# Kernel tuning notes

Measured on AMD Instinct MI355X. Metric: run time of the kernel, lower is better.

Reference implementation:

```python
import jax, jax.numpy as jnp
import numpy as np

B, S, D, E, K, O = 32, 2048, 1024, 16, 4, 1024


def setup_inputs() -> dict:
    key = jax.random.key(0)
    ks = jax.random.split(key, 9)
    sc = 0.02
    return {
        "x": jax.random.normal(ks[0], (B, S, D), dtype=jnp.float32),
        "Wg": jax.random.normal(ks[1], (D, E), dtype=jnp.float32) * sc,
        "bg": jnp.zeros((E,), dtype=jnp.float32),
        "W1": jax.random.normal(ks[2], (E, K * D, O), dtype=jnp.float32) * sc,
        "b1": jnp.zeros((E, O), dtype=jnp.float32),
        "W2": jax.random.normal(ks[3], (E, O, O), dtype=jnp.float32) * sc,
        "b2": jnp.zeros((E, O), dtype=jnp.float32),
        "W3": jax.random.normal(ks[4], (E, O, O), dtype=jnp.float32) * sc,
        "b3": jnp.zeros((E, O), dtype=jnp.float32),
    }


def reference(x, Wg, bg, W1, b1, W2, b2, W3, b3):
    b, s, d = x.shape
    e = Wg.shape[1]
    k = W1.shape[1] // d
    # gate logits [B,S,E]; softmax over the TOKEN axis (dim=-2 in torch)
    logits = jnp.einsum('bsd,de->bse', x, Wg) + bg
    probs = jax.nn.softmax(logits, axis=-2)          # [B,S,E]
    # top-k tokens per expert (torch.topk over dim=-2)
    vals, idx = jax.lax.top_k(probs.transpose(0, 2, 1), k)  # [B,E,k]
    # gather selected tokens: [B,E,k,D]
    tok = jnp.take_along_axis(x[:, None, :, :], idx[..., None], axis=2)
    # weight by gate prob, concat k tokens -> [B,E,k*D]
    inp = (tok * vals[..., None]).reshape(b, e, k * d)
    # per-expert 3-layer MLP as grouped GEMMs
    h = jax.nn.relu(jnp.einsum('bei,eio->beo', inp, W1) + b1)
    h = jax.nn.relu(jnp.einsum('beo,eop->bep', h, W2) + b2)
    out = jnp.einsum('beo,eop->bep', h, W3) + b3
    return out  # [B,E,O]
```

## Files before the change

kernel.cpp:

```cpp
#include <hip/hip_runtime.h>
#include <hip/hip_bf16.h>
#include <math.h>

constexpr int B = 32, S = 2048, D = 1024, E = 16, TK = 4, O = 1024;
constexpr int KD = TK * D;
constexpr int KS = 8;

__global__ __launch_bounds__(256) void k_logits(
    const float* __restrict__ x, const float* __restrict__ Wg,
    const float* __restrict__ bg, float* __restrict__ logitsT) {
  int row = blockIdx.x * 256 + threadIdx.x;
  int b = row / S, s = row % S;
  const float* xr = x + (size_t)row * D;
  float acc[E];
#pragma unroll
  for (int e = 0; e < E; e++) acc[e] = 0.f;
  for (int k = 0; k < D; k += 4) {
    float4 xv = *(const float4*)(xr + k);
    const float* w0 = Wg + (size_t)k * E;
#pragma unroll
    for (int e = 0; e < E; e++) {
      acc[e] += xv.x * w0[e] + xv.y * w0[E + e] + xv.z * w0[2 * E + e] +
                xv.w * w0[3 * E + e];
    }
  }
#pragma unroll
  for (int e = 0; e < E; e++)
    logitsT[((size_t)b * E + e) * S + s] = acc[e] + bg[e];
}

__global__ __launch_bounds__(256) void k_topk(
    const float* __restrict__ logitsT, int* __restrict__ tIdx,
    float* __restrict__ tVal) {
  int be = blockIdx.x;
  const float* lrow = logitsT + (size_t)be * S;
  __shared__ float sv[S];
  __shared__ float red[256];
  __shared__ int redi[256];
  int t = threadIdx.x;
  for (int i = t; i < S; i += 256) sv[i] = lrow[i];
  __syncthreads();
  float m = -1e30f;
  for (int i = t; i < S; i += 256) m = fmaxf(m, sv[i]);
  red[t] = m;
  __syncthreads();
  for (int off = 128; off > 0; off >>= 1) {
    if (t < off) red[t] = fmaxf(red[t], red[t + off]);
    __syncthreads();
  }
  float gmax = red[0];
  __syncthreads();
  float se = 0.f;
  for (int i = t; i < S; i += 256) se += expf(sv[i] - gmax);
  red[t] = se;
  __syncthreads();
  for (int off = 128; off > 0; off >>= 1) {
    if (t < off) red[t] += red[t + off];
    __syncthreads();
  }
  float sumexp = red[0];
  __syncthreads();
  for (int j = 0; j < 4; j++) {
    float bv = -1e30f;
    int bi = S;
    for (int i = t; i < S; i += 256) {
      float v = sv[i];
      if (v > bv || (v == bv && i < bi)) { bv = v; bi = i; }
    }
    red[t] = bv;
    redi[t] = bi;
    __syncthreads();
    for (int off = 128; off > 0; off >>= 1) {
      if (t < off) {
        float v2 = red[t + off];
        int i2 = redi[t + off];
        if (v2 > red[t] || (v2 == red[t] && i2 < redi[t])) {
          red[t] = v2;
          redi[t] = i2;
        }
      }
      __syncthreads();
    }
    if (t == 0) {
      tIdx[be * TK + j] = redi[0];
      tVal[be * TK + j] = expf(red[0] - gmax) / sumexp;
      sv[redi[0]] = -1e30f;
    }
    __syncthreads();
  }
}

__global__ __launch_bounds__(256) void k_gather(
    const float* __restrict__ x, const int* __restrict__ tIdx,
    const float* __restrict__ tVal, float* __restrict__ inpT) {
  int ej = blockIdx.x;
  int e = ej / TK, j = ej % TK;
  int d0 = blockIdx.y * 256;
  __shared__ float st[32][257];
  int tid = threadIdx.x;
  int dt = tid % 64;
  int bq = tid / 64;
  for (int bi = 0; bi < 8; bi++) {
    int b = bq * 8 + bi;
    int row = tIdx[(b * E + e) * TK + j];
    float v = tVal[(b * E + e) * TK + j];
    float4 xv = *(const float4*)(x + ((size_t)b * S + row) * D + d0 + dt * 4);
    st[b][dt * 4 + 0] = xv.x * v;
    st[b][dt * 4 + 1] = xv.y * v;
    st[b][dt * 4 + 2] = xv.z * v;
    st[b][dt * 4 + 3] = xv.w * v;
  }
  __syncthreads();
  size_t base = ((size_t)e * TK + j) * D + d0;
  for (int c = 0; c < 32; c++) {
    int idx = c * 256 + tid;
    int drel = idx / 32, b = idx % 32;
    inpT[(base + drel) * 32 + b] = st[b][drel];
  }
}

template <int KC>
__global__ __launch_bounds__(64) void k_gemm_part(
    const float* __restrict__ AT,
    const float* __restrict__ W,
    float* __restrict__ part,
    int Ktot) {
  int e = blockIdx.x, nt = blockIdx.y, ks = blockIdx.z;
  int n = nt * 64 + threadIdx.x;
  int k0 = ks * KC;
  const float* a = AT + ((size_t)e * Ktot + k0) * 32;
  const float* w = W + ((size_t)e * Ktot + k0) * O + n;
  float acc[32];
#pragma unroll
  for (int m = 0; m < 32; m++) acc[m] = 0.f;
#pragma unroll 4
  for (int k = 0; k < KC; k++) {
    float bv = w[(size_t)k * O];
    const float* ar = a + k * 32;
#pragma unroll
    for (int m = 0; m < 32; m++) acc[m] += ar[m] * bv;
  }
  float4* po4 = (float4*)(part + (((size_t)ks * E + e) * O + n) * 32);
#pragma unroll
  for (int q = 0; q < 8; q++)
    po4[q] = make_float4(acc[4 * q], acc[4 * q + 1], acc[4 * q + 2], acc[4 * q + 3]);
}

__global__ __launch_bounds__(256) void k_reduce_act(
    const float* __restrict__ part, const float* __restrict__ bias,
    float* __restrict__ outT, int relu) {
  size_t g = (size_t)blockIdx.x * 256 + threadIdx.x;
  const size_t stride4 = (size_t)E * O * 32 / 4;
  const float4* p4 = (const float4*)part;
  float4 s = p4[g];
#pragma unroll
  for (int ks = 1; ks < KS; ks++) {
    float4 v = p4[(size_t)ks * stride4 + g];
    s.x += v.x; s.y += v.y; s.z += v.z; s.w += v.w;
  }
  size_t el = g * 4;
  int n = (int)((el / 32) % O);
  int e = (int)(el / ((size_t)32 * O));
  float bv = bias[e * O + n];
  s.x += bv; s.y += bv; s.z += bv; s.w += bv;
  if (relu) {
    s.x = fmaxf(s.x, 0.f); s.y = fmaxf(s.y, 0.f);
    s.z = fmaxf(s.z, 0.f); s.w = fmaxf(s.w, 0.f);
  }
  ((float4*)outT)[g] = s;
}

__global__ __launch_bounds__(256) void k_final(
    const float* __restrict__ part, const float* __restrict__ bias,
    float* __restrict__ out) {
  int e = blockIdx.x;
  int o0 = blockIdx.y * 64;
  __shared__ float sd[64][33];
  int tid = threadIdx.x;
  const size_t stride = (size_t)E * O * 32;
  for (int c = 0; c < 8; c++) {
    int idx = c * 256 + tid;
    int orel = idx / 32, b = idx % 32;
    size_t off = ((size_t)e * O + o0 + orel) * 32 + b;
    float s = part[off];
#pragma unroll
    for (int ks = 1; ks < KS; ks++) s += part[(size_t)ks * stride + off];
    sd[orel][b] = s + bias[e * O + o0 + orel];
  }
  __syncthreads();
  for (int c = 0; c < 8; c++) {
    int idx = c * 256 + tid;
    int b = idx / 64, orr = idx % 64;
    out[((size_t)b * E + e) * O + o0 + orr] = sd[orr][b];
  }
}

extern "C" void kernel_launch(void* const* d_in, const int* in_sizes, int n_in,
                              void* d_out, int out_size, void* d_ws,
                              size_t ws_size, hipStream_t stream) {
  (void)in_sizes; (void)n_in; (void)out_size; (void)ws_size;
  const float* x  = (const float*)d_in[0];
  const float* Wg = (const float*)d_in[1];
  const float* bg = (const float*)d_in[2];
  const float* W1 = (const float*)d_in[3];
  const float* b1 = (const float*)d_in[4];
  const float* W2 = (const float*)d_in[5];
  const float* b2 = (const float*)d_in[6];
  const float* W3 = (const float*)d_in[7];
  const float* b3 = (const float*)d_in[8];
  float* out = (float*)d_out;

  char* ws = (char*)d_ws;
  float* logitsT = (float*)ws;
  int*   tIdx    = (int*)(ws + (4u << 20));
  float* tVal    = (float*)(ws + (4u << 20) + (8u << 10));
  float* inpT    = (float*)(ws + (4u << 20) + (64u << 10));
  float* part    = (float*)(ws + (12u << 20) + (64u << 10));
  float* h1T     = (float*)(ws + (28u << 20) + (64u << 10));
  float* h2T     = (float*)(ws + (30u << 20) + (64u << 10));

  k_logits<<<B * S / 256, 256, 0, stream>>>(x, Wg, bg, logitsT);
  k_topk<<<B * E, 256, 0, stream>>>(logitsT, tIdx, tVal);
  k_gather<<<dim3(E * TK, D / 256), 256, 0, stream>>>(x, tIdx, tVal, inpT);
  k_gemm_part<KD / KS><<<dim3(E, O / 64, KS), 64, 0, stream>>>(inpT, W1, part, KD);
  k_reduce_act<<<(E * O * 32 / 4) / 256, 256, 0, stream>>>(part, b1, h1T, 1);
  k_gemm_part<O / KS><<<dim3(E, O / 64, KS), 64, 0, stream>>>(h1T, W2, part, O);
  k_reduce_act<<<(E * O * 32 / 4) / 256, 256, 0, stream>>>(part, b2, h2T, 1);
  k_gemm_part<O / KS><<<dim3(E, O / 64, KS), 64, 0, stream>>>(h2T, W3, part, O);
  k_final<<<dim3(E, O / 64), 256, 0, stream>>>(part, b3, out);
}
```

Before: 847.6 us.

## Split logits K across waves and retile expert GEMM for vector weight loads

The gate-logit kernel now gives each of four waves a quarter of the feature dimension for 64 rows. It batches eight float4 loads of x per iteration and reduces the partial sums through shared memory. This raises memory-level parallelism on the large x read. The expert GEMM moves from 64-thread blocks, where each thread handled one output column and all 32 batch rows, to 256-thread blocks. Each thread now computes 4 columns by 8 rows using float4 weight loads unrolled by eight, which quarters the grid size and changes occupancy and register use.

```diff
diff --git a/kernel.cpp b/kernel.cpp
--- a/kernel.cpp
+++ b/kernel.cpp
@@ -9,24 +9,43 @@
 __global__ __launch_bounds__(256) void k_logits(
     const float* __restrict__ x, const float* __restrict__ Wg,
     const float* __restrict__ bg, float* __restrict__ logitsT) {
-  int row = blockIdx.x * 256 + threadIdx.x;
-  int b = row / S, s = row % S;
-  const float* xr = x + (size_t)row * D;
+  int tid = threadIdx.x;
+  int lane = tid & 63;
+  int wid = __builtin_amdgcn_readfirstlane(tid >> 6);
+  int row0 = blockIdx.x * 64;
+  int row = row0 + lane;
+  const float* xr = x + (size_t)row * D + wid * 256;
+  const float* wg = Wg + (size_t)wid * 256 * E;
   float acc[E];
 #pragma unroll
   for (int e = 0; e < E; e++) acc[e] = 0.f;
-  for (int k = 0; k < D; k += 4) {
-    float4 xv = *(const float4*)(xr + k);
-    const float* w0 = Wg + (size_t)k * E;
-#pragma unroll
-    for (int e = 0; e < E; e++) {
-      acc[e] += xv.x * w0[e] + xv.y * w0[E + e] + xv.z * w0[2 * E + e] +
-                xv.w * w0[3 * E + e];
-    }
-  }
-#pragma unroll
-  for (int e = 0; e < E; e++)
-    logitsT[((size_t)b * E + e) * S + s] = acc[e] + bg[e];
+  for (int it = 0; it < 64; it += 8) {
+    float4 xv[8];
+#pragma unroll
+    for (int u = 0; u < 8; u++)
+      xv[u] = *(const float4*)(xr + (it + u) * 4);
+#pragma unroll
+    for (int u = 0; u < 8; u++) {
+      const float* w0 = wg + (size_t)(it + u) * 4 * E;
+#pragma unroll
+      for (int e = 0; e < E; e++)
+        acc[e] += xv[u].x * w0[e] + xv[u].y * w0[E + e] +
+                  xv[u].z * w0[2 * E + e] + xv[u].w * w0[3 * E + e];
+    }
+  }
+  __shared__ float red[4][64][17];
+#pragma unroll
+  for (int e = 0; e < E; e++) red[wid][lane][e] = acc[e];
+  __syncthreads();
+  int b = row0 >> 11;
+  int s0 = row0 & (S - 1);
+#pragma unroll
+  for (int i = 0; i < 4; i++) {
+    int e = wid + i * 4;
+    float v = red[0][lane][e] + red[1][lane][e] + red[2][lane][e] +
+              red[3][lane][e] + bg[e];
+    logitsT[((size_t)b * E + e) * S + s0 + lane] = v;
+  }
 }
 
 __global__ __launch_bounds__(256) void k_topk(
@@ -120,30 +139,50 @@
 }
 
 template <int KC>
-__global__ __launch_bounds__(64) void k_gemm_part(
+__global__ __launch_bounds__(256) void k_gemm_part(
     const float* __restrict__ AT,
     const float* __restrict__ W,
     float* __restrict__ part,
     int Ktot) {
   int e = blockIdx.x, nt = blockIdx.y, ks = blockIdx.z;
-  int n = nt * 64 + threadIdx.x;
+  int tid = threadIdx.x;
+  int lane = tid & 63;
+  int m0 = __builtin_amdgcn_readfirstlane((tid >> 6) * 8);
+  int n0 = nt * 256 + lane * 4;
   int k0 = ks * KC;
-  const float* a = AT + ((size_t)e * Ktot + k0) * 32;
-  const float* w = W + ((size_t)e * Ktot + k0) * O + n;
-  float acc[32];
-#pragma unroll
-  for (int m = 0; m < 32; m++) acc[m] = 0.f;
-#pragma unroll 4
-  for (int k = 0; k < KC; k++) {
-    float bv = w[(size_t)k * O];
-    const float* ar = a + k * 32;
-#pragma unroll
-    for (int m = 0; m < 32; m++) acc[m] += ar[m] * bv;
-  }
-  float4* po4 = (float4*)(part + (((size_t)ks * E + e) * O + n) * 32);
-#pragma unroll
-  for (int q = 0; q < 8; q++)
-    po4[q] = make_float4(acc[4 * q], acc[4 * q + 1], acc[4 * q + 2], acc[4 * q + 3]);
+  const float* a = AT + ((size_t)e * Ktot + k0) * 32 + m0;
+  const float* w = W + ((size_t)e * Ktot + k0) * O + n0;
+  float acc[8][4];
+#pragma unroll
+  for (int m = 0; m < 8; m++)
+#pragma unroll
+    for (int q = 0; q < 4; q++) acc[m][q] = 0.f;
+  for (int k = 0; k < KC; k += 8) {
+    float4 wv[8];
+#pragma unroll
+    for (int u = 0; u < 8; u++)
+      wv[u] = *(const float4*)(w + (size_t)(k + u) * O);
+#pragma unroll
+    for (int u = 0; u < 8; u++) {
+      const float* ar = a + (size_t)(k + u) * 32;
+#pragma unroll
+      for (int m = 0; m < 8; m++) {
+        float av = ar[m];
+        acc[m][0] += av * wv[u].x;
+        acc[m][1] += av * wv[u].y;
+        acc[m][2] += av * wv[u].z;
+        acc[m][3] += av * wv[u].w;
+      }
+    }
+  }
+  float* pb = part + (((size_t)ks * E + e) * O + n0) * 32 + m0;
+#pragma unroll
+  for (int ni = 0; ni < 4; ni++) {
+    *(float4*)(pb + ni * 32) =
+        make_float4(acc[0][ni], acc[1][ni], acc[2][ni], acc[3][ni]);
+    *(float4*)(pb + ni * 32 + 4) =
+        make_float4(acc[4][ni], acc[5][ni], acc[6][ni], acc[7][ni]);
+  }
 }
 
 __global__ __launch_bounds__(256) void k_reduce_act(
@@ -219,13 +258,13 @@
   float* h1T     = (float*)(ws + (28u << 20) + (64u << 10));
   float* h2T     = (float*)(ws + (30u << 20) + (64u << 10));
 
-  k_logits<<<B * S / 256, 256, 0, stream>>>(x, Wg, bg, logitsT);
+  k_logits<<<B * S / 64, 256, 0, stream>>>(x, Wg, bg, logitsT);
   k_topk<<<B * E, 256, 0, stream>>>(logitsT, tIdx, tVal);
   k_gather<<<dim3(E * TK, D / 256), 256, 0, stream>>>(x, tIdx, tVal, inpT);
-  k_gemm_part<KD / KS><<<dim3(E, O / 64, KS), 64, 0, stream>>>(inpT, W1, part, KD);
+  k_gemm_part<KD / KS><<<dim3(E, O / 256, KS), 256, 0, stream>>>(inpT, W1, part, KD);
   k_reduce_act<<<(E * O * 32 / 4) / 256, 256, 0, stream>>>(part, b1, h1T, 1);
-  k_gemm_part<O / KS><<<dim3(E, O / 64, KS), 64, 0, stream>>>(h1T, W2, part, O);
+  k_gemm_part<O / KS><<<dim3(E, O / 256, KS), 256, 0, stream>>>(h1T, W2, part, O);
   k_reduce_act<<<(E * O * 32 / 4) / 256, 256, 0, stream>>>(part, b2, h2T, 1);
-  k_gemm_part<O / KS><<<dim3(E, O / 64, KS), 64, 0, stream>>>(h2T, W3, part, O);
+  k_gemm_part<O / KS><<<dim3(E, O / 256, KS), 256, 0, stream>>>(h2T, W3, part, O);
   k_final<<<dim3(E, O / 64), 256, 0, stream>>>(part, b3, out);
 }
```

Result: faster. 765.1 us (-9.7%).
